# Kernel tuning notes

Hardware: AMD Instinct MI355X
Metric: run time of the kernel (lower is better)

## Reference

```python
import jax, jax.numpy as jnp
import numpy as np
from jax.scipy.special import betaln

B, T = 4096, 8192

def setup_inputs() -> dict:
    key = jax.random.key(0)
    k_obs, k_a1, k_b1, k_a2, k_b2 = jax.random.split(key, 5)
    obs_seq = (jax.random.uniform(k_obs, (B, T)) < 0.5).astype(jnp.float32)
    # priors strictly positive, away from 0 to keep betaln finite
    alpha1 = jax.random.uniform(k_a1, (B,)) * 2.0 + 0.5
    beta1 = jax.random.uniform(k_b1, (B,)) * 2.0 + 0.5
    alpha2 = jax.random.uniform(k_a2, (B,)) * 2.0 + 0.5
    beta2 = jax.random.uniform(k_b2, (B,)) * 2.0 + 0.5
    mixweight = jnp.float32(0.4)
    return {"obs_seq": obs_seq, "alpha1": alpha1, "beta1": beta1,
            "alpha2": alpha2, "beta2": beta2, "mixweight": mixweight}

def reference(obs_seq, alpha1, beta1, alpha2, beta2, mixweight):
    # cumulative successes/failures, shifted right by one (posterior BEFORE obs t)
    cs = jnp.cumsum(obs_seq, axis=1)          # [B,T]
    cf = jnp.cumsum(1.0 - obs_seq, axis=1)    # [B,T]
    s_prev = jnp.pad(cs[:, :-1], ((0, 0), (1, 0)))  # cat([0, cs[:-1]])
    f_prev = jnp.pad(cf[:, :-1], ((0, 0), (1, 0)))
    a1 = alpha1[:, None] + s_prev
    b1 = beta1[:, None] + f_prev
    a2 = alpha2[:, None] + s_prev
    b2 = beta2[:, None] + f_prev
    clog1 = betaln(a1, b1) - betaln(alpha1, beta1)[:, None]
    clog2 = betaln(a2, b2) - betaln(alpha2, beta2)[:, None]
    bigconst = -clog1
    c1 = mixweight * jnp.exp(clog1 + bigconst)
    c2 = (1.0 - mixweight) * jnp.exp(clog2 + bigconst)
    post_mixweight = c1 / (c1 + c2)
    # stack the post_dict entries into one [5,B,T] array
    return jnp.stack([a1, b1, a2, b2, post_mixweight])
```

## Files before the change

### kernel.cpp

```cpp
#include <hip/hip_runtime.h>


#define BLOCK 256

__global__ __launch_bounds__(BLOCK) void bbm_kernel(
    const float* __restrict__ obs,
    const float* __restrict__ alpha1, const float* __restrict__ beta1,
    const float* __restrict__ alpha2, const float* __restrict__ beta2,
    const float* __restrict__ mixw,
    float* __restrict__ out,
    int T, size_t bt_stride)
{
    const int row  = blockIdx.x;
    const int tid  = threadIdx.x;
    const int lane = tid & 63;
    const int wid  = tid >> 6;

    __shared__ int   sPart[4];
    __shared__ float dPart[4];

    const float A1 = alpha1[row], B1 = beta1[row];
    const float A2 = alpha2[row], B2 = beta2[row];
    const float w  = mixw[0];
    const float AB1 = A1 + B1, AB2 = A2 + B2;
    const float w2 = 1.0f - w;

    const float* __restrict__ orow = obs + (size_t)row * T;
    float* __restrict__ obase = out + (size_t)row * T;

    int   carry_s = 0;
    float carry_d = 0.0f;

    const int segs = T / BLOCK;
    for (int seg = 0; seg < segs; ++seg) {
        const int t = seg * BLOCK + tid;
        const float ov = orow[t];
        const int bit = (ov > 0.5f) ? 1 : 0;

        int incl_s = bit;
        #pragma unroll
        for (int off = 1; off < 64; off <<= 1) {
            int n = __shfl_up(incl_s, off, 64);
            if (lane >= off) incl_s += n;
        }
        if (lane == 63) sPart[wid] = incl_s;
        __syncthreads();
        int prior_s = 0, total_s = 0;
        #pragma unroll
        for (int wI = 0; wI < 4; ++wI) {
            int p = sPart[wI];
            total_s += p;
            if (wI < wid) prior_s += p;
        }
        const int s_prev = carry_s + prior_s + (incl_s - bit);

        const float ft     = (float)t;
        const float fs     = (float)s_prev;
        const float f_prev = ft - fs;
        const float a1v = A1 + fs,     b1v = B1 + f_prev;
        const float a2v = A2 + fs,     b2v = B2 + f_prev;
        const float sel1 = bit ? a1v : b1v;
        const float sel2 = bit ? a2v : b2v;
        const float delta = __logf(sel2 * (AB1 + ft)) - __logf(sel1 * (AB2 + ft));

        float incl_d = delta;
        #pragma unroll
        for (int off = 1; off < 64; off <<= 1) {
            float n = __shfl_up(incl_d, off, 64);
            if (lane >= off) incl_d += n;
        }
        if (lane == 63) dPart[wid] = incl_d;
        __syncthreads();
        float prior_d = 0.0f, total_d = 0.0f;
        #pragma unroll
        for (int wI = 0; wI < 4; ++wI) {
            float p = dPart[wI];
            total_d += p;
            if (wI < wid) prior_d += p;
        }
        const float d = carry_d + prior_d + (incl_d - delta);

        const float e  = __expf(d);
        const float pm = w / (w + w2 * e);

        obase[t]                 = a1v;
        obase[t +     bt_stride] = b1v;
        obase[t + 2 * bt_stride] = a2v;
        obase[t + 3 * bt_stride] = b2v;
        obase[t + 4 * bt_stride] = pm;

        carry_s += total_s;
        carry_d += total_d;
    }
}

extern "C" void kernel_launch(void* const* d_in, const int* in_sizes, int n_in,
                              void* d_out, int out_size, void* d_ws, size_t ws_size,
                              hipStream_t stream) {
    const float* obs    = (const float*)d_in[0];
    const float* alpha1 = (const float*)d_in[1];
    const float* beta1  = (const float*)d_in[2];
    const float* alpha2 = (const float*)d_in[3];
    const float* beta2  = (const float*)d_in[4];
    const float* mixw   = (const float*)d_in[5];

    const int Bn = in_sizes[1];
    const int Tn = in_sizes[0] / Bn;
    const size_t bt = (size_t)Bn * (size_t)Tn;

    bbm_kernel<<<Bn, BLOCK, 0, stream>>>(obs, alpha1, beta1, alpha2, beta2,
                                         mixw, (float*)d_out, Tn, bt);
}
```

Measured before the change: 764.6 us.

## Process eight elements per thread with serial local scan and vector stores

Each thread now handles eight consecutive timesteps. It loads them with 128-bit vector loads, does a serial local prefix sum, and runs one wave/block scan per 2048-element segment instead of per 256. Outputs are written as float4 nontemporal stores. This cuts shuffle and barrier overhead per element and widens memory transactions. It raises register use, and the kernel still uses one block per row.

```diff
diff --git a/kernel.cpp b/kernel.cpp
--- a/kernel.cpp
+++ b/kernel.cpp
@@ -2,6 +2,9 @@
 
 
 #define BLOCK 256
+#define VEC 8
+
+typedef float v4f __attribute__((ext_vector_type(4)));
 
 __global__ __launch_bounds__(BLOCK) void bbm_kernel(
     const float* __restrict__ obs,
@@ -9,7 +12,7 @@
     const float* __restrict__ alpha2, const float* __restrict__ beta2,
     const float* __restrict__ mixw,
     float* __restrict__ out,
-    int T, size_t bt_stride)
+    int T, size_t bt)
 {
     const int row  = blockIdx.x;
     const int tid  = threadIdx.x;
@@ -31,39 +34,53 @@
     int   carry_s = 0;
     float carry_d = 0.0f;
 
-    const int segs = T / BLOCK;
+    const int EPB  = BLOCK * VEC;
+    const int segs = T / EPB;
+
     for (int seg = 0; seg < segs; ++seg) {
-        const int t = seg * BLOCK + tid;
-        const float ov = orow[t];
-        const int bit = (ov > 0.5f) ? 1 : 0;
+        const int t0 = seg * EPB + tid * VEC;
 
-        int incl_s = bit;
+        v4f o0 = *(const v4f*)(orow + t0);
+        v4f o1 = *(const v4f*)(orow + t0 + 4);
+        float ov[VEC] = {o0.x, o0.y, o0.z, o0.w, o1.x, o1.y, o1.z, o1.w};
+
+        int bit[VEC], sloc[VEC];
+        int ts = 0;
+        #pragma unroll
+        for (int j = 0; j < VEC; ++j) { bit[j] = ov[j] > 0.5f; sloc[j] = ts; ts += bit[j]; }
+
+        int incl = ts;
         #pragma unroll
         for (int off = 1; off < 64; off <<= 1) {
-            int n = __shfl_up(incl_s, off, 64);
-            if (lane >= off) incl_s += n;
+            int n = __shfl_up(incl, off, 64);
+            if (lane >= off) incl += n;
         }
-        if (lane == 63) sPart[wid] = incl_s;
+        if (lane == 63) sPart[wid] = incl;
         __syncthreads();
-        int prior_s = 0, total_s = 0;
+        int prior = 0, total = 0;
         #pragma unroll
         for (int wI = 0; wI < 4; ++wI) {
             int p = sPart[wI];
-            total_s += p;
-            if (wI < wid) prior_s += p;
+            total += p;
+            if (wI < wid) prior += p;
         }
-        const int s_prev = carry_s + prior_s + (incl_s - bit);
+        const int tbase_s = carry_s + prior + (incl - ts);
 
-        const float ft     = (float)t;
-        const float fs     = (float)s_prev;
-        const float f_prev = ft - fs;
-        const float a1v = A1 + fs,     b1v = B1 + f_prev;
-        const float a2v = A2 + fs,     b2v = B2 + f_prev;
-        const float sel1 = bit ? a1v : b1v;
-        const float sel2 = bit ? a2v : b2v;
-        const float delta = __logf(sel2 * (AB1 + ft)) - __logf(sel1 * (AB2 + ft));
+        float dloc[VEC];
+        float td = 0.0f;
+        #pragma unroll
+        for (int j = 0; j < VEC; ++j) {
+            const float ft = (float)(t0 + j);
+            const float fs = (float)(tbase_s + sloc[j]);
+            const float fp = ft - fs;
+            const float sel1 = bit[j] ? (A1 + fs) : (B1 + fp);
+            const float sel2 = bit[j] ? (A2 + fs) : (B2 + fp);
+            const float delta = __logf(sel2 * (AB1 + ft)) - __logf(sel1 * (AB2 + ft));
+            dloc[j] = td;
+            td += delta;
+        }
 
-        float incl_d = delta;
+        float incl_d = td;
         #pragma unroll
         for (int off = 1; off < 64; off <<= 1) {
             float n = __shfl_up(incl_d, off, 64);
@@ -71,26 +88,42 @@
         }
         if (lane == 63) dPart[wid] = incl_d;
         __syncthreads();
-        float prior_d = 0.0f, total_d = 0.0f;
+        float priord = 0.0f, totald = 0.0f;
         #pragma unroll
         for (int wI = 0; wI < 4; ++wI) {
             float p = dPart[wI];
-            total_d += p;
-            if (wI < wid) prior_d += p;
+            totald += p;
+            if (wI < wid) priord += p;
         }
-        const float d = carry_d + prior_d + (incl_d - delta);
+        const float tbase_d = carry_d + priord + (incl_d - td);
 
-        const float e  = __expf(d);
-        const float pm = w / (w + w2 * e);
+        #pragma unroll
+        for (int h = 0; h < VEC / 4; ++h) {
+            v4f va1, vb1, va2, vb2, vpm;
+            #pragma unroll
+            for (int j = 0; j < 4; ++j) {
+                const int e  = h * 4 + j;
+                const float ft = (float)(t0 + e);
+                const float fs = (float)(tbase_s + sloc[e]);
+                const float fp = ft - fs;
+                const float d  = tbase_d + dloc[e];
+                const float pm = w / (w + w2 * __expf(d));
+                va1[j] = A1 + fs;
+                vb1[j] = B1 + fp;
+                va2[j] = A2 + fs;
+                vb2[j] = B2 + fp;
+                vpm[j] = pm;
+            }
+            float* p = obase + t0 + h * 4;
+            __builtin_nontemporal_store(va1, (v4f*)(p));
+            __builtin_nontemporal_store(vb1, (v4f*)(p + bt));
+            __builtin_nontemporal_store(va2, (v4f*)(p + 2 * bt));
+            __builtin_nontemporal_store(vb2, (v4f*)(p + 3 * bt));
+            __builtin_nontemporal_store(vpm, (v4f*)(p + 4 * bt));
+        }
 
-        obase[t]                 = a1v;
-        obase[t +     bt_stride] = b1v;
-        obase[t + 2 * bt_stride] = a2v;
-        obase[t + 3 * bt_stride] = b2v;
-        obase[t + 4 * bt_stride] = pm;
-
-        carry_s += total_s;
-        carry_d += total_d;
+        carry_s += total;
+        carry_d += totald;
     }
 }
 
```

Result: slower. 1.138 ms (+48.8%).
